# Optimization experiments

Measured on AMD Instinct MI355X. Metric: run time of the kernel, lower is better.

Reference implementation:

```python
import jax, jax.numpy as jnp
import numpy as np

E = 100   # embedding_dim (Config)
H = 256   # hidden_dim (Config)


def setup_inputs() -> dict:
    key = jax.random.key(0)
    ks = jax.random.split(key, 16)
    V, T = 30000, 20
    B, L = 128, 512
    s = 0.05
    w = lambda k, shape: jax.random.normal(k, shape, dtype=jnp.float32) * s
    return {
        "sentences": jax.random.randint(ks[0], (B, L), 0, V, dtype=jnp.int32),
        "tags": jax.random.randint(ks[1], (B, L), 0, T, dtype=jnp.int32),
        "mask": jnp.ones((B, L), dtype=bool),
        "emb": w(ks[2], (V, E)),
        "Wih_f": w(ks[3], (4 * H, E)), "Whh_f": w(ks[4], (4 * H, H)),
        "bih_f": w(ks[5], (4 * H,)),   "bhh_f": w(ks[6], (4 * H,)),
        "Wih_b": w(ks[7], (4 * H, E)), "Whh_b": w(ks[8], (4 * H, H)),
        "bih_b": w(ks[9], (4 * H,)),   "bhh_b": w(ks[10], (4 * H,)),
        "Wout": w(ks[11], (T, 2 * H)), "bout": w(ks[12], (T,)),
        "trans": w(ks[13], (T, T)),
        "start_t": w(ks[14], (T,)),
        "end_t": w(ks[15], (T,)),
    }


def _lstm_dir(x, Wih, Whh, bih, bhh):
    # x: [B, L, E]; PyTorch gate order i, f, g, o; h0 = c0 = 0.
    B = x.shape[0]
    Hd = Whh.shape[1]
    b = bih + bhh

    def step(carry, xt):
        h, c = carry
        g = xt @ Wih.T + h @ Whh.T + b                      # [B, 4H]
        i, f, gg, o = jnp.split(g, 4, axis=-1)
        c = jax.nn.sigmoid(f) * c + jax.nn.sigmoid(i) * jnp.tanh(gg)
        h = jax.nn.sigmoid(o) * jnp.tanh(c)
        return (h, c), h

    init = (jnp.zeros((B, Hd), x.dtype), jnp.zeros((B, Hd), x.dtype))
    _, hs = jax.lax.scan(step, init, jnp.swapaxes(x, 0, 1))    # [L, B, H]
    return jnp.swapaxes(hs, 0, 1)


def _crf_nll(emissions, tags, mask, trans, start_t, end_t):
    # torchcrf log-likelihood with reduction='sum'; returns |-(llh)|.
    B, L, T = emissions.shape
    maskf = mask.astype(emissions.dtype)
    em_t = jnp.swapaxes(emissions, 0, 1)   # [L, B, T]
    tg_t = jnp.swapaxes(tags, 0, 1)        # [L, B]
    mk_t = jnp.swapaxes(maskf, 0, 1)       # [L, B]
    bidx = jnp.arange(B)

    # --- gold path score ---
    score0 = start_t[tags[:, 0]] + emissions[bidx, 0, tags[:, 0]]

    def score_step(s, inp):
        prev, cur, m, em = inp
        s = s + (trans[prev, cur] + em[bidx, cur]) * m
        return s, None

    score, _ = jax.lax.scan(score_step, score0,
                            (tg_t[:-1], tg_t[1:], mk_t[1:], em_t[1:]))
    seq_ends = mask.sum(axis=1).astype(jnp.int32) - 1
    last_tags = tags[bidx, seq_ends]
    score = score + end_t[last_tags]

    # --- log partition (forward algorithm) ---
    def alpha_step(a, inp):
        m, em = inp
        nxt = jax.nn.logsumexp(a[:, :, None] + trans[None] + em[:, None, :], axis=1)
        return jnp.where(m[:, None] > 0, nxt, a), None

    a0 = start_t[None, :] + em_t[0]
    alpha, _ = jax.lax.scan(alpha_step, a0, (mk_t[1:], em_t[1:]))
    logZ = jax.nn.logsumexp(alpha + end_t[None, :], axis=1)

    llh = jnp.sum(score - logZ)
    return jnp.abs(-llh)  # loss.mean() on a scalar is identity


def reference(sentences, tags, mask, emb, Wih_f, Whh_f, bih_f, bhh_f,
              Wih_b, Whh_b, bih_b, bhh_b, Wout, bout, trans, start_t, end_t):
    x = emb[sentences]                                           # [B, L, E]
    h_f = _lstm_dir(x, Wih_f, Whh_f, bih_f, bhh_f)               # [B, L, H]
    h_b = _lstm_dir(x[:, ::-1], Wih_b, Whh_b, bih_b, bhh_b)[:, ::-1]
    lstm_out = jnp.concatenate([h_f, h_b], axis=-1)              # [B, L, 2H]
    emissions = lstm_out @ Wout.T + bout                         # [B, L, T]
    return _crf_nll(emissions, tags, mask, trans, start_t, end_t)
```

## Files before the change

### kernel.cpp

```cpp
#include <hip/hip_runtime.h>


typedef float f32x4 __attribute__((ext_vector_type(4)));

#define MFMAF8(a, b, c) \
  __builtin_amdgcn_mfma_f32_16x16x32_fp8_fp8((a), (b), (c), 0, 0, 0)
#define ATOMIC_LD(p) __hip_atomic_load((p), __ATOMIC_RELAXED, __HIP_MEMORY_SCOPE_AGENT)
#define ATOMIC_ST(p, v) \
  __hip_atomic_store((p), (v), __ATOMIC_RELAXED, __HIP_MEMORY_SCOPE_AGENT)

__device__ __forceinline__ unsigned short f2bf(float x) {
  unsigned u = __float_as_uint(x);
  u += 0x7FFFu + ((u >> 16) & 1u);
  return (unsigned short)(u >> 16);
}
__device__ __forceinline__ float bf2f(unsigned short h) {
  return __uint_as_float(((unsigned)h) << 16);
}
__device__ __forceinline__ float sigm(float x) {
  return __builtin_amdgcn_rcpf(1.f + __expf(-x));
}
__device__ __forceinline__ float tanh_(float x) {
  float e = __expf(2.f * x);
  return (e - 1.f) * __builtin_amdgcn_rcpf(e + 1.f);
}
__device__ __forceinline__ unsigned pack_fp8x4(float a, float b, float c, float d) {
  int p = __builtin_amdgcn_cvt_pk_fp8_f32(a, b, 0, false);
  p = __builtin_amdgcn_cvt_pk_fp8_f32(c, d, p, true);
  return (unsigned)p;
}

__global__ __launch_bounds__(256) void prep_kernel(
    const float* __restrict__ Whh_f, const float* __restrict__ Whh_b,
    const float* __restrict__ Wih_f, const float* __restrict__ Wih_b,
    const float* __restrict__ Wout,
    const float* __restrict__ bih_f, const float* __restrict__ bhh_f,
    const float* __restrict__ bih_b, const float* __restrict__ bhh_b,
    long* __restrict__ whh, long* __restrict__ wih, long* __restrict__ wout,
    float* __restrict__ bias, int* __restrict__ flags) {
  int bid = blockIdx.x, tid = threadIdx.x;
  if (bid < 256) {
    int gid = bid * 256 + tid;
    int l = gid & 63, kt = (gid >> 6) & 7, n = (gid >> 9) & 63, dir = gid >> 15;
    const float* src = dir ? Whh_b : Whh_f;
    int row = n * 16 + (l & 15), k0 = kt * 32 + ((l >> 4) << 3);
    float v[8];
#pragma unroll
    for (int e = 0; e < 8; ++e) v[e] = src[row * 256 + k0 + e];
    unsigned lo = pack_fp8x4(v[0], v[1], v[2], v[3]);
    unsigned hi = pack_fp8x4(v[4], v[5], v[6], v[7]);
    whh[gid] = (long)lo | ((long)hi << 32);
  } else if (bid < 384) {
    int gid = (bid - 256) * 256 + tid;
    int l = gid & 63, kt = (gid >> 6) & 3, n = (gid >> 8) & 63, dir = gid >> 14;
    const float* src = dir ? Wih_b : Wih_f;
    int row = n * 16 + (l & 15), k0 = kt * 32 + ((l >> 4) << 3);
    float v[8];
#pragma unroll
    for (int e = 0; e < 8; ++e) {
      int k = k0 + e;
      v[e] = (k < 100) ? src[row * 100 + k] : 0.f;
    }
    unsigned lo = pack_fp8x4(v[0], v[1], v[2], v[3]);
    unsigned hi = pack_fp8x4(v[4], v[5], v[6], v[7]);
    wih[gid] = (long)lo | ((long)hi << 32);
  } else if (bid < 392) {
    int gid = (bid - 384) * 256 + tid;
    if (gid < 2048) {
      int l = gid & 63, kt = (gid >> 6) & 7, n = (gid >> 9) & 1, dir = gid >> 10;
      int colt = n * 16 + (l & 15), k0 = kt * 32 + ((l >> 4) << 3);
      float v[8];
#pragma unroll
      for (int e = 0; e < 8; ++e)
        v[e] = (colt < 20) ? Wout[colt * 512 + dir * 256 + k0 + e] : 0.f;
      unsigned lo = pack_fp8x4(v[0], v[1], v[2], v[3]);
      unsigned hi = pack_fp8x4(v[4], v[5], v[6], v[7]);
      wout[gid] = (long)lo | ((long)hi << 32);
    }
  } else if (bid < 400) {
    int idx = (bid - 392) * 256 + tid;
    if (idx < 2048) {
      int dir = idx >> 10, c = idx & 1023;
      bias[idx] = dir ? (bih_b[c] + bhh_b[c]) : (bih_f[c] + bhh_f[c]);
    }
  } else {
    if (tid < 64) flags[tid] = 0;
  }
}

__global__ __launch_bounds__(512) void lstm_kernel(
    const int* __restrict__ sent, const float* __restrict__ emb,
    const long* __restrict__ whh, const long* __restrict__ wih,
    const long* __restrict__ wout, const float* __restrict__ bias,
    float* __restrict__ em_out, unsigned char* __restrict__ h_glob,
    int* __restrict__ flags)
{
  __shared__ long whh_lds[16][8][64];
  __shared__ long wih_lds[16][4][64];
  __shared__ unsigned char h_lds[16][272];
  __shared__ unsigned char x_lds[2][16][136];
  __shared__ unsigned short g_T[256][18];
  __shared__ long wout_lds[2][8][64];
  __shared__ float bias_lds[256];

  const int tid = threadIdx.x;
  const int lid = tid & 63, w = tid >> 6;
  const int p = blockIdx.x & 15, q = blockIdx.x >> 4;
  const int dir = p >> 3, bt = p & 7, r0 = bt * 16;

  const int arow = lid & 15;
  const int aq = lid >> 4;
  const int rb = aq * 4;
  const int g = w >> 1, s = w & 1;
  const int li0 = g * 4 + s * 2, li1 = li0 + 1;

  {
    const long* whh_d = whh + dir * 32768;
    for (int idx = tid; idx < 8192; idx += 512) {
      int li = idx >> 9, rem = idx & 511, kt = rem >> 6, ln = rem & 63;
      int nt = (li >> 2) * 16 + q * 4 + (li & 3);
      (&whh_lds[0][0][0])[idx] = whh_d[(nt * 8 + kt) * 64 + ln];
    }
    const long* wih_d = wih + dir * 16384;
    for (int idx = tid; idx < 4096; idx += 512) {
      int li = idx >> 8, rem = idx & 255, kt = rem >> 6, ln = rem & 63;
      int nt = (li >> 2) * 16 + q * 4 + (li & 3);
      (&wih_lds[0][0][0])[idx] = wih_d[(nt * 4 + kt) * 64 + ln];
    }
    const long* wo_d = wout + dir * 1024;
    ((long*)wout_lds)[tid] = wo_d[tid];
    ((long*)wout_lds)[tid + 512] = wo_d[tid + 512];
    if (tid < 256) {
      int li = tid >> 4, r = tid & 15;
      int nt = (li >> 2) * 16 + q * 4 + (li & 3);
      bias_lds[tid] = bias[dir * 1024 + nt * 16 + r];
    }
  }
  for (int i = tid; i < 16 * 272; i += 512) ((unsigned char*)h_lds)[i] = 0;
  for (int i = tid; i < 2 * 16 * 136; i += 512) ((unsigned char*)x_lds)[i] = 0;

  const int ur = tid & 15, jb = (tid >> 4) * 2;
  float creg[2];
  creg[0] = 0.f;
  creg[1] = 0.f;

  unsigned* hb0 = (unsigned*)(h_glob + p * 4096);
  unsigned* hb1 = (unsigned*)(h_glob + 65536 + p * 4096);
  int* fl = flags + p * 4;

  const int pqa = (q + 1) & 3, pqb = (q + 2) & 3, pqc = (q + 3) & 3;
  const int prow = (tid & 255) >> 4, pwi = tid & 15;
  const bool roleA = (tid < 256);

  const int rxA = tid / 25, cxA = tid - rxA * 25;
  const bool hasX = (tid < 400);

  if (hasX) {
    int t0 = dir ? 511 : 0;
    int sid = sent[(r0 + rxA) * 512 + t0];
    float4 v = *(const float4*)&emb[sid * 100 + cxA * 4];
    *(unsigned*)&x_lds[0][rxA][cxA * 4] = pack_fp8x4(v.x, v.y, v.z, v.w);
  }
  __syncthreads();

  for (int t = 0; t < 512; ++t) {
    float4 xN;
    const bool haveN = hasX && (t < 511);
    if (haveN) {
      int te = dir ? (511 - (t + 1)) : (t + 1);
      int sid = sent[(r0 + rxA) * 512 + te];
      xN = *(const float4*)&emb[sid * 100 + cxA * 4];
    }

    unsigned wa = 0, wb2 = 0, wc = 0;
    if (t > 0) {
      if (tid < 3) {
        int pq = (q + 1 + tid) & 3;
        while (ATOMIC_LD(&fl[pq]) < t) __builtin_amdgcn_s_sleep(2);
      }
      __syncthreads();
      unsigned* srcw = (t & 1) ? hb0 : hb1;
      if (roleA) {
        wa = ATOMIC_LD(&srcw[prow * 64 + pqa * 16 + pwi]);
        wc = ATOMIC_LD(&srcw[prow * 64 + pqc * 16 + pwi]);
      } else {
        wb2 = ATOMIC_LD(&srcw[prow * 64 + pqb * 16 + pwi]);
      }
    }

    const unsigned char(*xb)[136] = (const unsigned char(*)[136])x_lds[t & 1];

    f32x4 acc0, acc1;
    {
      float b0 = bias_lds[li0 * 16 + arow], b1 = bias_lds[li1 * 16 + arow];
      f32x4 a0 = {b0, b0, b0, b0}, a1 = {b1, b1, b1, b1};
      acc0 = a0;
      acc1 = a1;
    }
#pragma unroll
    for (int j = 0; j < 2; ++j) {
      int kt = 2 * q + j;
      long a8 = *(const long*)&h_lds[arow][kt * 32 + aq * 8];
      acc0 = MFMAF8(a8, whh_lds[li0][kt][lid], acc0);
      acc1 = MFMAF8(a8, whh_lds[li1][kt][lid], acc1);
    }
#pragma unroll
    for (int kt = 0; kt < 4; ++kt) {
      long a8 = *(const long*)&xb[arow][kt * 32 + aq * 8];
      acc0 = MFMAF8(a8, wih_lds[li0][kt][lid], acc0);
      acc1 = MFMAF8(a8, wih_lds[li1][kt][lid], acc1);
    }

    if (t > 0) {
      if (roleA) {
        *(unsigned*)&h_lds[prow][pqa * 64 + pwi * 4] = wa;
        *(unsigned*)&h_lds[prow][pqc * 64 + pwi * 4] = wc;
      } else {
        *(unsigned*)&h_lds[prow][pqb * 64 + pwi * 4] = wb2;
      }
    }
    __syncthreads();

#pragma unroll
    for (int j = 2; j < 8; ++j) {
      int kt = (2 * q + j) & 7;
      long a8 = *(const long*)&h_lds[arow][kt * 32 + aq * 8];
      acc0 = MFMAF8(a8, whh_lds[li0][kt][lid], acc0);
      acc1 = MFMAF8(a8, whh_lds[li1][kt][lid], acc1);
    }
    {
      int lcol0 = li0 * 16 + arow, lcol1 = li1 * 16 + arow;
      *(unsigned*)&g_T[lcol0][rb] =
          (unsigned)f2bf(acc0[0]) | ((unsigned)f2bf(acc0[1]) << 16);
      *(unsigned*)&g_T[lcol0][rb + 2] =
          (unsigned)f2bf(acc0[2]) | ((unsigned)f2bf(acc0[3]) << 16);
      *(unsigned*)&g_T[lcol1][rb] =
          (unsigned)f2bf(acc1[0]) | ((unsigned)f2bf(acc1[1]) << 16);
      *(unsigned*)&g_T[lcol1][rb + 2] =
          (unsigned)f2bf(acc1[2]) | ((unsigned)f2bf(acc1[3]) << 16);
    }

    if (t > 0 && w == 0 && (q == 1 || q == 2)) {
      int nt = q - 1;
      f32x4 e = {0.f, 0.f, 0.f, 0.f};
#pragma unroll
      for (int kt = 0; kt < 8; ++kt) {
        long a8 = *(const long*)&h_lds[arow][kt * 32 + aq * 8];
        e = MFMAF8(a8, wout_lds[nt][kt][lid], e);
      }
      int col = nt * 16 + arow;
      if (col < 20) {
        int tp = dir ? (512 - t) : (t - 1);
        int base = ((dir * 128 + r0 + rb) * 512 + tp) * 20 + col;
#pragma unroll
        for (int r = 0; r < 4; ++r) em_out[base + r * 10240] = e[r];
      }
    }
    __syncthreads();

    {
      float hv[2];
#pragma unroll
      for (int j = 0; j < 2; ++j) {
        int c = jb + j;
        float xi = bf2f(g_T[c][ur]);
        float xf = bf2f(g_T[64 + c][ur]);
        float xg = bf2f(g_T[128 + c][ur]);
        float xo = bf2f(g_T[192 + c][ur]);
        float cc = sigm(xf) * creg[j] + sigm(xi) * tanh_(xg);
        creg[j] = cc;
        hv[j] = sigm(xo) * tanh_(cc);
      }
      unsigned pk =
          (unsigned)__builtin_amdgcn_cvt_pk_fp8_f32(hv[0], hv[1], 0, false);
      *(unsigned short*)&h_lds[ur][q * 64 + jb] = (unsigned short)pk;
      unsigned short* dst16 =
          (unsigned short*)((t & 1) ? hb1 : hb0);
      ATOMIC_ST(&dst16[ur * 128 + ((q * 64 + jb) >> 1)], (unsigned short)pk);
    }
    if (haveN) {
      *(unsigned*)&x_lds[(t + 1) & 1][rxA][cxA * 4] =
          pack_fp8x4(xN.x, xN.y, xN.z, xN.w);
    }
    __syncthreads();
    if (tid == 0) ATOMIC_ST(&fl[q], t + 1);
  }

  if (q == 1 || q == 2) {
    if (tid < 3) {
      int pq = (q + 1 + tid) & 3;
      while (ATOMIC_LD(&fl[pq]) < 512) __builtin_amdgcn_s_sleep(2);
    }
    __syncthreads();
    if (roleA) {
      unsigned wa2 = ATOMIC_LD(&hb1[prow * 64 + pqa * 16 + pwi]);
      unsigned wc2 = ATOMIC_LD(&hb1[prow * 64 + pqc * 16 + pwi]);
      *(unsigned*)&h_lds[prow][pqa * 64 + pwi * 4] = wa2;
      *(unsigned*)&h_lds[prow][pqc * 64 + pwi * 4] = wc2;
    } else {
      unsigned wb3 = ATOMIC_LD(&hb1[prow * 64 + pqb * 16 + pwi]);
      *(unsigned*)&h_lds[prow][pqb * 64 + pwi * 4] = wb3;
    }
    __syncthreads();
    if (w == 0) {
      int nt = q - 1;
      f32x4 e = {0.f, 0.f, 0.f, 0.f};
#pragma unroll
      for (int kt = 0; kt < 8; ++kt) {
        long a8 = *(const long*)&h_lds[arow][kt * 32 + aq * 8];
        e = MFMAF8(a8, wout_lds[nt][kt][lid], e);
      }
      int col = nt * 16 + arow;
      if (col < 20) {
        int tp = dir ? 0 : 511;
        int base = ((dir * 128 + r0 + rb) * 512 + tp) * 20 + col;
#pragma unroll
        for (int r = 0; r < 4; ++r) em_out[base + r * 10240] = e[r];
      }
    }
  }
}

__global__ __launch_bounds__(64) void crf_kernel(
    const float* __restrict__ emf, const float* __restrict__ embk,
    const int* __restrict__ tags, const int* __restrict__ maski,
    const float* __restrict__ bout, const float* __restrict__ trans,
    const float* __restrict__ start_t, const float* __restrict__ end_t,
    float* __restrict__ partial) {
  __shared__ float tr[400];
  const int b = blockIdx.x, tid = threadIdx.x;
  for (int i = tid; i < 400; i += 64) tr[i] = trans[i];
  __syncthreads();

  const int tp = tid;
  const bool act = tp < 20;
  float eT[20];
  if (act) {
#pragma unroll
    for (int t2 = 0; t2 < 20; ++t2) eT[t2] = __expf(tr[t2 * 20 + tp]);
  }
  const float* ef = emf + (size_t)b * 10240;
  const float* eb = embk + (size_t)b * 10240;
  const float bo = act ? bout[tp] : 0.f;

  float a = act ? (start_t[tp] + ef[tp] + eb[tp] + bo) : -1e30f;

  float efn = 0.f, ebn = 0.f;
  if (act) { efn = ef[20 + tp]; ebn = eb[20 + tp]; }

  for (int l = 1; l < 512; ++l) {
    float e_cur = efn + ebn + bo;
    if (act && l + 1 < 512) { efn = ef[(l + 1) * 20 + tp]; ebn = eb[(l + 1) * 20 + tp]; }
    float m = a;
#pragma unroll
    for (int o = 16; o > 0; o >>= 1) m = fmaxf(m, __shfl_xor(m, o, 32));
    float pv = __expf(a - m);
    float sgm = 0.f;
#pragma unroll
    for (int t2 = 0; t2 < 20; ++t2) sgm += __shfl(pv, t2, 32) * eT[t2];
    float anew = m + __logf(sgm) + e_cur;
    int mk = maski[b * 512 + l];
    if (act && mk) a = anew;
  }
  float v = act ? (a + end_t[tp]) : -1e30f;
  float m2 = v;
#pragma unroll
  for (int o = 16; o > 0; o >>= 1) m2 = fmaxf(m2, __shfl_xor(m2, o, 32));
  float s2 = __expf(v - m2);
#pragma unroll
  for (int o = 16; o > 0; o >>= 1) s2 += __shfl_xor(s2, o, 32);
  float logZ = m2 + __logf(s2);

  const int* tg = tags + b * 512;
  float sc = 0.f;
  int cnt = 0;
  for (int l = tid; l < 512; l += 64) {
    int mk = maski[b * 512 + l];
    cnt += mk ? 1 : 0;
    if (l >= 1 && mk) {
      int cur = tg[l], prev = tg[l - 1];
      sc += tr[prev * 20 + cur] + ef[l * 20 + cur] + eb[l * 20 + cur] + bout[cur];
    }
  }
#pragma unroll
  for (int o = 32; o > 0; o >>= 1) {
    sc += __shfl_xor(sc, o, 64);
    cnt += __shfl_xor(cnt, o, 64);
  }
  if (tid == 0) {
    int t0 = tg[0];
    sc += start_t[t0] + ef[t0] + eb[t0] + bout[t0];
    sc += end_t[tg[cnt - 1]];
    partial[b] = sc - logZ;
  }
}

__global__ __launch_bounds__(64) void final_kernel(const float* __restrict__ partial,
                                                   float* __restrict__ out) {
  int tid = threadIdx.x;
  float s = partial[tid] + partial[tid + 64];
#pragma unroll
  for (int o = 32; o > 0; o >>= 1) s += __shfl_xor(s, o, 64);
  if (tid == 0) out[0] = fabsf(s);
}

extern "C" void kernel_launch(void* const* d_in, const int* in_sizes, int n_in,
                              void* d_out, int out_size, void* d_ws, size_t ws_size,
                              hipStream_t stream) {
  const int* sent = (const int*)d_in[0];
  const int* tags = (const int*)d_in[1];
  const int* maski = (const int*)d_in[2];
  const float* emb = (const float*)d_in[3];
  const float* Wih_f = (const float*)d_in[4];
  const float* Whh_f = (const float*)d_in[5];
  const float* bih_f = (const float*)d_in[6];
  const float* bhh_f = (const float*)d_in[7];
  const float* Wih_b = (const float*)d_in[8];
  const float* Whh_b = (const float*)d_in[9];
  const float* bih_b = (const float*)d_in[10];
  const float* bhh_b = (const float*)d_in[11];
  const float* Wout = (const float*)d_in[12];
  const float* bout = (const float*)d_in[13];
  const float* trans = (const float*)d_in[14];
  const float* start_t = (const float*)d_in[15];
  const float* end_t = (const float*)d_in[16];

  char* ws = (char*)d_ws;
  float* em_base = (float*)ws;
  float* em_f = em_base;
  float* em_b = em_base + 128 * 512 * 20;
  long* whh_f8 = (long*)(ws + 10485760);
  long* wih_f8 = (long*)(ws + 11010048);
  long* wout_f8 = (long*)(ws + 11272192);
  float* bias_d = (float*)(ws + 11288576);
  float* partial = (float*)(ws + 11296768);
  int* flags = (int*)(ws + 11297280);
  unsigned char* h_glob = (unsigned char*)(ws + 11300864);

  prep_kernel<<<401, 256, 0, stream>>>(Whh_f, Whh_b, Wih_f, Wih_b, Wout,
                                       bih_f, bhh_f, bih_b, bhh_b,
                                       whh_f8, wih_f8, wout_f8, bias_d, flags);
  lstm_kernel<<<64, 512, 0, stream>>>(sent, emb, whh_f8, wih_f8, wout_f8,
                                      bias_d, em_base, h_glob, flags);
  crf_kernel<<<128, 64, 0, stream>>>(em_f, em_b, tags, maski, bout, trans,
                                     start_t, end_t, partial);
  final_kernel<<<1, 64, 0, stream>>>(partial, (float*)d_out);
}
```

Baseline: 1.360 ms.

## Split each LSTM recurrence across 8 cooperating blocks instead of 4

Doubles the lstm_kernel grid from 64 to 128 blocks, so each batch-tile/direction group is handled by 8 blocks that each own 32 hidden units, down from 64. Each wave now does one MFMA chain rather than two, and the cell update uses one column per thread with a shuffle to pack fp8 pairs. This shortens per-step compute on the serial critical path. In exchange every block must wait on 7 peer flags per timestep and gather more remote h fragments, so synchronisation and exchange costs grow.

```diff
diff --git a/kernel.cpp b/kernel.cpp
--- a/kernel.cpp
+++ b/kernel.cpp
@@ -84,7 +84,7 @@
       bias[idx] = dir ? (bih_b[c] + bhh_b[c]) : (bih_f[c] + bhh_f[c]);
     }
   } else {
-    if (tid < 64) flags[tid] = 0;
+    if (tid < 128) flags[tid] = 0;
   }
 }
 
@@ -95,62 +95,62 @@
     float* __restrict__ em_out, unsigned char* __restrict__ h_glob,
     int* __restrict__ flags)
 {
-  __shared__ long whh_lds[16][8][64];
-  __shared__ long wih_lds[16][4][64];
+  __shared__ long whh_lds[8][8][64];
+  __shared__ long wih_lds[8][4][64];
   __shared__ unsigned char h_lds[16][272];
   __shared__ unsigned char x_lds[2][16][136];
-  __shared__ unsigned short g_T[256][18];
+  __shared__ unsigned short g_T[128][18];
   __shared__ long wout_lds[2][8][64];
-  __shared__ float bias_lds[256];
+  __shared__ float bias_lds[128];
 
   const int tid = threadIdx.x;
   const int lid = tid & 63, w = tid >> 6;
-  const int p = blockIdx.x & 15, q = blockIdx.x >> 4;
+  const int p = blockIdx.x & 15, o = blockIdx.x >> 4;
   const int dir = p >> 3, bt = p & 7, r0 = bt * 16;
 
   const int arow = lid & 15;
   const int aq = lid >> 4;
   const int rb = aq * 4;
-  const int g = w >> 1, s = w & 1;
-  const int li0 = g * 4 + s * 2, li1 = li0 + 1;
 
   {
     const long* whh_d = whh + dir * 32768;
-    for (int idx = tid; idx < 8192; idx += 512) {
+    for (int idx = tid; idx < 4096; idx += 512) {
       int li = idx >> 9, rem = idx & 511, kt = rem >> 6, ln = rem & 63;
-      int nt = (li >> 2) * 16 + q * 4 + (li & 3);
+      int nt = (li >> 1) * 16 + o * 2 + (li & 1);
       (&whh_lds[0][0][0])[idx] = whh_d[(nt * 8 + kt) * 64 + ln];
     }
     const long* wih_d = wih + dir * 16384;
-    for (int idx = tid; idx < 4096; idx += 512) {
+    for (int idx = tid; idx < 2048; idx += 512) {
       int li = idx >> 8, rem = idx & 255, kt = rem >> 6, ln = rem & 63;
-      int nt = (li >> 2) * 16 + q * 4 + (li & 3);
+      int nt = (li >> 1) * 16 + o * 2 + (li & 1);
       (&wih_lds[0][0][0])[idx] = wih_d[(nt * 4 + kt) * 64 + ln];
     }
     const long* wo_d = wout + dir * 1024;
     ((long*)wout_lds)[tid] = wo_d[tid];
     ((long*)wout_lds)[tid + 512] = wo_d[tid + 512];
-    if (tid < 256) {
+    if (tid < 128) {
       int li = tid >> 4, r = tid & 15;
-      int nt = (li >> 2) * 16 + q * 4 + (li & 3);
+      int nt = (li >> 1) * 16 + o * 2 + (li & 1);
       bias_lds[tid] = bias[dir * 1024 + nt * 16 + r];
     }
   }
   for (int i = tid; i < 16 * 272; i += 512) ((unsigned char*)h_lds)[i] = 0;
   for (int i = tid; i < 2 * 16 * 136; i += 512) ((unsigned char*)x_lds)[i] = 0;
 
-  const int ur = tid & 15, jb = (tid >> 4) * 2;
-  float creg[2];
-  creg[0] = 0.f;
-  creg[1] = 0.f;
+  const int ur = tid & 15, jc = tid >> 4;
+  float creg = 0.f;
 
   unsigned* hb0 = (unsigned*)(h_glob + p * 4096);
   unsigned* hb1 = (unsigned*)(h_glob + 65536 + p * 4096);
-  int* fl = flags + p * 4;
-
-  const int pqa = (q + 1) & 3, pqb = (q + 2) & 3, pqc = (q + 3) & 3;
-  const int prow = (tid & 255) >> 4, pwi = tid & 15;
-  const bool roleA = (tid < 256);
+  int* fl = flags + p * 8;
+
+  const int w0 = tid;
+  const int pj0 = w0 >> 7, rem0 = w0 & 127, row0 = rem0 >> 3, wq0 = rem0 & 7;
+  const int po0 = (o + 1 + pj0) & 7;
+  const int w1 = tid + 512;
+  const int pj1 = w1 >> 7, rem1 = w1 & 127, row1 = rem1 >> 3, wq1 = rem1 & 7;
+  const int po1 = (o + 1 + pj1) & 7;
+  const bool hasW1 = (tid < 384);
 
   const int rxA = tid / 25, cxA = tid - rxA * 25;
   const bool hasX = (tid < 400);
@@ -172,76 +172,58 @@
       xN = *(const float4*)&emb[sid * 100 + cxA * 4];
     }
 
-    unsigned wa = 0, wb2 = 0, wc = 0;
+    unsigned wa = 0, wb2 = 0;
     if (t > 0) {
-      if (tid < 3) {
-        int pq = (q + 1 + tid) & 3;
+      if (tid < 7) {
+        int pq = (o + 1 + tid) & 7;
         while (ATOMIC_LD(&fl[pq]) < t) __builtin_amdgcn_s_sleep(2);
       }
       __syncthreads();
       unsigned* srcw = (t & 1) ? hb0 : hb1;
-      if (roleA) {
-        wa = ATOMIC_LD(&srcw[prow * 64 + pqa * 16 + pwi]);
-        wc = ATOMIC_LD(&srcw[prow * 64 + pqc * 16 + pwi]);
-      } else {
-        wb2 = ATOMIC_LD(&srcw[prow * 64 + pqb * 16 + pwi]);
-      }
+      wa = ATOMIC_LD(&srcw[row0 * 64 + po0 * 8 + wq0]);
+      if (hasW1) wb2 = ATOMIC_LD(&srcw[row1 * 64 + po1 * 8 + wq1]);
     }
 
     const unsigned char(*xb)[136] = (const unsigned char(*)[136])x_lds[t & 1];
 
-    f32x4 acc0, acc1;
+    f32x4 acc;
     {
-      float b0 = bias_lds[li0 * 16 + arow], b1 = bias_lds[li1 * 16 + arow];
-      f32x4 a0 = {b0, b0, b0, b0}, a1 = {b1, b1, b1, b1};
-      acc0 = a0;
-      acc1 = a1;
-    }
-#pragma unroll
-    for (int j = 0; j < 2; ++j) {
-      int kt = 2 * q + j;
-      long a8 = *(const long*)&h_lds[arow][kt * 32 + aq * 8];
-      acc0 = MFMAF8(a8, whh_lds[li0][kt][lid], acc0);
-      acc1 = MFMAF8(a8, whh_lds[li1][kt][lid], acc1);
+      float bb = bias_lds[w * 16 + arow];
+      f32x4 a = {bb, bb, bb, bb};
+      acc = a;
+    }
+    {
+      long a8 = *(const long*)&h_lds[arow][o * 32 + aq * 8];
+      acc = MFMAF8(a8, whh_lds[w][o][lid], acc);
     }
 #pragma unroll
     for (int kt = 0; kt < 4; ++kt) {
       long a8 = *(const long*)&xb[arow][kt * 32 + aq * 8];
-      acc0 = MFMAF8(a8, wih_lds[li0][kt][lid], acc0);
-      acc1 = MFMAF8(a8, wih_lds[li1][kt][lid], acc1);
+      acc = MFMAF8(a8, wih_lds[w][kt][lid], acc);
     }
 
     if (t > 0) {
-      if (roleA) {
-        *(unsigned*)&h_lds[prow][pqa * 64 + pwi * 4] = wa;
-        *(unsigned*)&h_lds[prow][pqc * 64 + pwi * 4] = wc;
-      } else {
-        *(unsigned*)&h_lds[prow][pqb * 64 + pwi * 4] = wb2;
-      }
+      *(unsigned*)&h_lds[row0][po0 * 32 + wq0 * 4] = wa;
+      if (hasW1) *(unsigned*)&h_lds[row1][po1 * 32 + wq1 * 4] = wb2;
     }
     __syncthreads();
 
 #pragma unroll
-    for (int j = 2; j < 8; ++j) {
-      int kt = (2 * q + j) & 7;
+    for (int j = 1; j < 8; ++j) {
+      int kt = (o + j) & 7;
       long a8 = *(const long*)&h_lds[arow][kt * 32 + aq * 8];
-      acc0 = MFMAF8(a8, whh_lds[li0][kt][lid], acc0);
-      acc1 = MFMAF8(a8, whh_lds[li1][kt][lid], acc1);
+      acc = MFMAF8(a8, whh_lds[w][kt][lid], acc);
     }
     {
-      int lcol0 = li0 * 16 + arow, lcol1 = li1 * 16 + arow;
-      *(unsigned*)&g_T[lcol0][rb] =
-          (unsigned)f2bf(acc0[0]) | ((unsigned)f2bf(acc0[1]) << 16);
-      *(unsigned*)&g_T[lcol0][rb + 2] =
-          (unsigned)f2bf(acc0[2]) | ((unsigned)f2bf(acc0[3]) << 16);
-      *(unsigned*)&g_T[lcol1][rb] =
-          (unsigned)f2bf(acc1[0]) | ((unsigned)f2bf(acc1[1]) << 16);
-      *(unsigned*)&g_T[lcol1][rb + 2] =
-          (unsigned)f2bf(acc1[2]) | ((unsigned)f2bf(acc1[3]) << 16);
-    }
-
-    if (t > 0 && w == 0 && (q == 1 || q == 2)) {
-      int nt = q - 1;
+      int lcol = w * 16 + arow;
+      *(unsigned*)&g_T[lcol][rb] =
+          (unsigned)f2bf(acc[0]) | ((unsigned)f2bf(acc[1]) << 16);
+      *(unsigned*)&g_T[lcol][rb + 2] =
+          (unsigned)f2bf(acc[2]) | ((unsigned)f2bf(acc[3]) << 16);
+    }
+
+    if (t > 0 && w == 0 && (o == 1 || o == 2)) {
+      int nt = o - 1;
       f32x4 e = {0.f, 0.f, 0.f, 0.f};
 #pragma unroll
       for (int kt = 0; kt < 8; ++kt) {
@@ -259,51 +241,48 @@
     __syncthreads();
 
     {
-      float hv[2];
-#pragma unroll
-      for (int j = 0; j < 2; ++j) {
-        int c = jb + j;
-        float xi = bf2f(g_T[c][ur]);
-        float xf = bf2f(g_T[64 + c][ur]);
-        float xg = bf2f(g_T[128 + c][ur]);
-        float xo = bf2f(g_T[192 + c][ur]);
-        float cc = sigm(xf) * creg[j] + sigm(xi) * tanh_(xg);
-        creg[j] = cc;
-        hv[j] = sigm(xo) * tanh_(cc);
-      }
-      unsigned pk =
-          (unsigned)__builtin_amdgcn_cvt_pk_fp8_f32(hv[0], hv[1], 0, false);
-      *(unsigned short*)&h_lds[ur][q * 64 + jb] = (unsigned short)pk;
-      unsigned short* dst16 =
-          (unsigned short*)((t & 1) ? hb1 : hb0);
-      ATOMIC_ST(&dst16[ur * 128 + ((q * 64 + jb) >> 1)], (unsigned short)pk);
+      float xi = bf2f(g_T[jc][ur]);
+      float xf = bf2f(g_T[32 + jc][ur]);
+      float xg = bf2f(g_T[64 + jc][ur]);
+      float xo = bf2f(g_T[96 + jc][ur]);
+      float cc = sigm(xf) * creg + sigm(xi) * tanh_(xg);
+      creg = cc;
+      float hv = sigm(xo) * tanh_(cc);
+      float hv2 = __shfl(hv, lid + 16, 64);
+      if ((jc & 1) == 0) {
+        unsigned pk =
+            (unsigned)__builtin_amdgcn_cvt_pk_fp8_f32(hv, hv2, 0, false);
+        *(unsigned short*)&h_lds[ur][o * 32 + jc] = (unsigned short)pk;
+        unsigned short* dst16 =
+            (unsigned short*)((t & 1) ? hb1 : hb0);
+        ATOMIC_ST(&dst16[ur * 128 + ((o * 32 + jc) >> 1)], (unsigned short)pk);
+      }
     }
     if (haveN) {
       *(unsigned*)&x_lds[(t + 1) & 1][rxA][cxA * 4] =
           pack_fp8x4(xN.x, xN.y, xN.z, xN.w);
     }
     __syncthreads();
-    if (tid == 0) ATOMIC_ST(&fl[q], t + 1);
-  }
-
-  if (q == 1 || q == 2) {
-    if (tid < 3) {
-      int pq = (q + 1 + tid) & 3;
+    if (tid == 0) ATOMIC_ST(&fl[o], t + 1);
+  }
+
+  if (o == 1 || o == 2) {
+    if (tid < 7) {
+      int pq = (o + 1 + tid) & 7;
       while (ATOMIC_LD(&fl[pq]) < 512) __builtin_amdgcn_s_sleep(2);
     }
     __syncthreads();
-    if (roleA) {
-      unsigned wa2 = ATOMIC_LD(&hb1[prow * 64 + pqa * 16 + pwi]);
-      unsigned wc2 = ATOMIC_LD(&hb1[prow * 64 + pqc * 16 + pwi]);
-      *(unsigned*)&h_lds[prow][pqa * 64 + pwi * 4] = wa2;
-      *(unsigned*)&h_lds[prow][pqc * 64 + pwi * 4] = wc2;
-    } else {
-      unsigned wb3 = ATOMIC_LD(&hb1[prow * 64 + pqb * 16 + pwi]);
-      *(unsigned*)&h_lds[prow][pqb * 64 + pwi * 4] = wb3;
+    {
+      unsigned wa2 = ATOMIC_LD(&hb1[row0 * 64 + po0 * 8 + wq0]);
+      *(unsigned*)&h_lds[row0][po0 * 32 + wq0 * 4] = wa2;
+      if (hasW1) {
+        unsigned wb3 = ATOMIC_LD(&hb1[row1 * 64 + po1 * 8 + wq1]);
+        *(unsigned*)&h_lds[row1][po1 * 32 + wq1 * 4] = wb3;
+      }
     }
     __syncthreads();
     if (w == 0) {
-      int nt = q - 1;
+      int nt = o - 1;
       f32x4 e = {0.f, 0.f, 0.f, 0.f};
 #pragma unroll
       for (int kt = 0; kt < 8; ++kt) {
@@ -353,7 +332,7 @@
     if (act && l + 1 < 512) { efn = ef[(l + 1) * 20 + tp]; ebn = eb[(l + 1) * 20 + tp]; }
     float m = a;
 #pragma unroll
-    for (int o = 16; o > 0; o >>= 1) m = fmaxf(m, __shfl_xor(m, o, 32));
+    for (int ofs = 16; ofs > 0; ofs >>= 1) m = fmaxf(m, __shfl_xor(m, ofs, 32));
     float pv = __expf(a - m);
     float sgm = 0.f;
 #pragma unroll
@@ -365,10 +344,10 @@
   float v = act ? (a + end_t[tp]) : -1e30f;
   float m2 = v;
 #pragma unroll
-  for (int o = 16; o > 0; o >>= 1) m2 = fmaxf(m2, __shfl_xor(m2, o, 32));
+  for (int ofs = 16; ofs > 0; ofs >>= 1) m2 = fmaxf(m2, __shfl_xor(m2, ofs, 32));
   float s2 = __expf(v - m2);
 #pragma unroll
-  for (int o = 16; o > 0; o >>= 1) s2 += __shfl_xor(s2, o, 32);
+  for (int ofs = 16; ofs > 0; ofs >>= 1) s2 += __shfl_xor(s2, ofs, 32);
   float logZ = m2 + __logf(s2);
 
   const int* tg = tags + b * 512;
@@ -383,9 +362,9 @@
     }
   }
 #pragma unroll
-  for (int o = 32; o > 0; o >>= 1) {
-    sc += __shfl_xor(sc, o, 64);
-    cnt += __shfl_xor(cnt, o, 64);
+  for (int ofs = 32; ofs > 0; ofs >>= 1) {
+    sc += __shfl_xor(sc, ofs, 64);
+    cnt += __shfl_xor(cnt, ofs, 64);
   }
   if (tid == 0) {
     int t0 = tg[0];
@@ -400,7 +379,7 @@
   int tid = threadIdx.x;
   float s = partial[tid] + partial[tid + 64];
 #pragma unroll
-  for (int o = 32; o > 0; o >>= 1) s += __shfl_xor(s, o, 64);
+  for (int ofs = 32; ofs > 0; ofs >>= 1) s += __shfl_xor(s, ofs, 64);
   if (tid == 0) out[0] = fabsf(s);
 }
 
@@ -440,8 +419,8 @@
   prep_kernel<<<401, 256, 0, stream>>>(Whh_f, Whh_b, Wih_f, Wih_b, Wout,
                                        bih_f, bhh_f, bih_b, bhh_b,
                                        whh_f8, wih_f8, wout_f8, bias_d, flags);
-  lstm_kernel<<<64, 512, 0, stream>>>(sent, emb, whh_f8, wih_f8, wout_f8,
-                                      bias_d, em_base, h_glob, flags);
+  lstm_kernel<<<128, 512, 0, stream>>>(sent, emb, whh_f8, wih_f8, wout_f8,
+                                       bias_d, em_base, h_glob, flags);
   crf_kernel<<<128, 64, 0, stream>>>(em_f, em_b, tags, maski, bout, trans,
                                      start_t, end_t, partial);
   final_kernel<<<1, 64, 0, stream>>>(partial, (float*)d_out);
```

New measurement: 1.255 ms (median of 2 runs). 7.7% less time.
